# Optimization experiments

Hardware: AMD Instinct MI355X
Metric: run time of the kernel (lower is better)

The kernel has to match this reference:

```python
import jax, jax.numpy as jnp
import numpy as np

B, L, E, H = 2, 2048, 512, 8
D = E // H  # head_dim = 64


def setup_inputs() -> dict:
    key = jax.random.key(0)
    ks = jax.random.split(key, 12)
    s = 0.02
    return {
        "values": jax.random.normal(ks[0], (B, L, E), jnp.float32),
        "keys": jax.random.normal(ks[1], (B, L, E), jnp.float32),
        "query": jax.random.normal(ks[2], (B, L, E), jnp.float32),
        "mask": jax.random.randint(ks[3], (B, 1, L, L), 0, 2, jnp.int32),
        "Wv": jax.random.normal(ks[4], (E, E), jnp.float32) * s,
        "bv": jax.random.normal(ks[5], (E,), jnp.float32) * s,
        "Wk": jax.random.normal(ks[6], (E, E), jnp.float32) * s,
        "bk": jax.random.normal(ks[7], (E,), jnp.float32) * s,
        "Wq": jax.random.normal(ks[8], (E, E), jnp.float32) * s,
        "bq": jax.random.normal(ks[9], (E,), jnp.float32) * s,
        "Wo": jax.random.normal(ks[10], (E, E), jnp.float32) * s,
        "bo": jax.random.normal(ks[11], (E,), jnp.float32) * s,
    }


def reference(values, keys, query, mask, Wv, bv, Wk, bk, Wq, bq, Wo, bo):
    b, lq = query.shape[0], query.shape[1]
    # torch Linear: y = x @ W.T + b
    v = (values @ Wv.T + bv).reshape(b, -1, H, D)
    k = (keys @ Wk.T + bk).reshape(b, -1, H, D)
    q = (query @ Wq.T + bq).reshape(b, lq, H, D)
    energy = jnp.einsum("bqhd,bkhd->bhqk", q, k)  # [B,H,Lq,Lk]
    # mask applied BEFORE the scale, as in the original
    energy = jnp.where(mask == 0, jnp.float32(-1e20), energy)
    # NOTE: scales by sqrt(embed_size), not sqrt(head_dim) (faithful)
    attn = jax.nn.softmax(energy / jnp.sqrt(jnp.float32(E)), axis=3)
    out = jnp.einsum("bhql,blhd->bqhd", attn, v).reshape(b, lq, E)
    return out @ Wo.T + bo
```

## Files before the change

kernel.cpp:

```cpp
#include <hip/hip_runtime.h>
#include <hip/hip_bf16.h>
#include <math.h>

#define BB 2
#define LL 2048
#define EE 512
#define HH 8
#define DD 64
#define MM (BB * LL)
#define LW (LL / 64)

typedef short bf16x8 __attribute__((ext_vector_type(8)));
typedef float f32x4 __attribute__((ext_vector_type(4)));

#define MFMA16(a, b, c) __builtin_amdgcn_mfma_f32_16x16x32_bf16((a), (b), (c), 0, 0, 0)

__device__ __forceinline__ void gl2lds16(const __hip_bfloat16* g, __hip_bfloat16* l) {
    __builtin_amdgcn_global_load_lds(
        (const __attribute__((address_space(1))) unsigned int*)(g),
        (__attribute__((address_space(3))) unsigned int*)(l),
        16, 0, 0);
}

__device__ __forceinline__ uint4 cvt8_bf16(const float4 a, const float4 b) {
    union { __hip_bfloat16 h[8]; uint4 u; } t;
    t.h[0] = __float2bfloat16(a.x); t.h[1] = __float2bfloat16(a.y);
    t.h[2] = __float2bfloat16(a.z); t.h[3] = __float2bfloat16(a.w);
    t.h[4] = __float2bfloat16(b.x); t.h[5] = __float2bfloat16(b.y);
    t.h[6] = __float2bfloat16(b.z); t.h[7] = __float2bfloat16(b.w);
    return t.u;
}

struct PrepArgs {
    const float* xsrc[3];
    __hip_bfloat16* xdst[3];
    const float* wsrc[4];
    __hip_bfloat16* wdst[4];
    const int* mask;
    unsigned long long* mbits;
};

__global__ __launch_bounds__(256) void prep(PrepArgs a) {
    const int blk = blockIdx.x;
    if (blk < 3072) {
        const int t = blk >> 10;
        const int i = ((blk & 1023) * 256 + threadIdx.x) * 8;
        const float* s = a.xsrc[t] + i;
        float4 f0 = *(const float4*)(s);
        float4 f1 = *(const float4*)(s + 4);
        *(uint4*)(a.xdst[t] + i) = cvt8_bf16(f0, f1);
    } else if (blk < 3584) {
        const int r = blk - 3072;
        const int t = r >> 7;
        const int i = ((r & 127) * 256 + threadIdx.x) * 8;
        const float* s = a.wsrc[t] + i;
        float4 f0 = *(const float4*)(s);
        float4 f1 = *(const float4*)(s + 4);
        *(uint4*)(a.wdst[t] + i) = cvt8_bf16(f0, f1);
    } else {
        const size_t idx = (size_t)(blk - 3584) * 256 + threadIdx.x;
        const int m = a.mask[idx];
        const unsigned long long w = __ballot(m != 0);
        if ((threadIdx.x & 63) == 0) a.mbits[idx >> 6] = w;
    }
}

__global__ __launch_bounds__(256) void transpose_v(
    const __hip_bfloat16* __restrict__ vb, __hip_bfloat16* __restrict__ vt) {
    __shared__ __hip_bfloat16 T[64][72];
    const int tid = threadIdx.x;
    const int l0 = blockIdx.x * 64;
    const int h = blockIdx.y;
    const int b = blockIdx.z;
    const int row = tid >> 2;
    const int cg = (tid & 3) * 16;

    const __hip_bfloat16* src = vb + ((size_t)b * LL + l0 + row) * EE + h * DD + cg;
    *(uint4*)&T[row][cg] = *(const uint4*)src;
    *(uint4*)&T[row][cg + 8] = *(const uint4*)(src + 8);
    __syncthreads();

    __hip_bfloat16 t[16];
    #pragma unroll
    for (int e = 0; e < 16; ++e) t[e] = T[cg + e][row];
    __hip_bfloat16* dst = vt + (((size_t)b * HH + h) * DD + row) * LL + l0 + cg;
    *(uint4*)&dst[0] = *(uint4*)&t[0];
    *(uint4*)&dst[8] = *(uint4*)&t[8];
}

struct QKVArgs {
    const __hip_bfloat16* X[3];
    const __hip_bfloat16* W[3];
    const float* bias[3];
    __hip_bfloat16* O[3];
};

__global__ __launch_bounds__(256) void gemm_qkv128(QKVArgs p) {
    __shared__ __hip_bfloat16 As[128 * 32];
    __shared__ __hip_bfloat16 Bs[128 * 32];

    const int z = blockIdx.z;
    const __hip_bfloat16* __restrict__ X = p.X[z];
    const __hip_bfloat16* __restrict__ W = p.W[z];
    const float* __restrict__ bias = p.bias[z];
    __hip_bfloat16* __restrict__ O = p.O[z];
    const float oscale = (z == 0) ? 0.04419417382415922f : 1.0f;

    const int tid = threadIdx.x;
    const int wave = tid >> 6, lane = tid & 63;
    const int l15 = lane & 15, quad = lane >> 4;
    const int wm = (wave >> 1) * 64, wn = (wave & 1) * 64;
    const int m0 = blockIdx.y * 128, n0 = blockIdx.x * 128;

    const int srow = wave * 32 + (lane >> 2);
    const int scol = (lane & 3) * 8;
    const __hip_bfloat16* Ag = X + (size_t)(m0 + srow) * EE + scol;
    const __hip_bfloat16* Bg = W + (size_t)(n0 + srow) * EE + scol;
    __hip_bfloat16* Al = As + wave * 32 * 32;
    __hip_bfloat16* Bl = Bs + wave * 32 * 32;

    f32x4 acc[4][4] = {};

    for (int k0 = 0; k0 < EE; k0 += 32) {
        gl2lds16(Ag + k0, Al);
        gl2lds16(Ag + k0 + (size_t)16 * EE, Al + 16 * 32);
        gl2lds16(Bg + k0, Bl);
        gl2lds16(Bg + k0 + (size_t)16 * EE, Bl + 16 * 32);
        __syncthreads();

        bf16x8 af[4], bfr[4];
        #pragma unroll
        for (int i = 0; i < 4; ++i)
            af[i] = *(const bf16x8*)&As[(wm + i * 16 + l15) * 32 + quad * 8];
        #pragma unroll
        for (int j = 0; j < 4; ++j)
            bfr[j] = *(const bf16x8*)&Bs[(wn + j * 16 + l15) * 32 + quad * 8];
        #pragma unroll
        for (int i = 0; i < 4; ++i)
            #pragma unroll
            for (int j = 0; j < 4; ++j)
                acc[i][j] = MFMA16(af[i], bfr[j], acc[i][j]);
        __syncthreads();
    }

    #pragma unroll
    for (int i = 0; i < 4; ++i)
        #pragma unroll
        for (int j = 0; j < 4; ++j) {
            const int n = n0 + wn + j * 16 + l15;
            const float bv = bias[n];
            #pragma unroll
            for (int reg = 0; reg < 4; ++reg) {
                const int m = m0 + wm + i * 16 + quad * 4 + reg;
                O[(size_t)m * EE + n] = __float2bfloat16((acc[i][j][reg] + bv) * oscale);
            }
        }
}

__global__ __launch_bounds__(256) void gemm_out128(
    const __hip_bfloat16* __restrict__ X, const __hip_bfloat16* __restrict__ W,
    const float* __restrict__ bias, float* __restrict__ C) {
    __shared__ __hip_bfloat16 As[128 * 32];
    __shared__ __hip_bfloat16 Bs[128 * 32];

    const int tid = threadIdx.x;
    const int wave = tid >> 6, lane = tid & 63;
    const int l15 = lane & 15, quad = lane >> 4;
    const int wm = (wave >> 1) * 64, wn = (wave & 1) * 64;
    const int m0 = blockIdx.y * 128, n0 = blockIdx.x * 128;

    const int srow = wave * 32 + (lane >> 2);
    const int scol = (lane & 3) * 8;
    const __hip_bfloat16* Ag = X + (size_t)(m0 + srow) * EE + scol;
    const __hip_bfloat16* Bg = W + (size_t)(n0 + srow) * EE + scol;
    __hip_bfloat16* Al = As + wave * 32 * 32;
    __hip_bfloat16* Bl = Bs + wave * 32 * 32;

    f32x4 acc[4][4] = {};

    for (int k0 = 0; k0 < EE; k0 += 32) {
        gl2lds16(Ag + k0, Al);
        gl2lds16(Ag + k0 + (size_t)16 * EE, Al + 16 * 32);
        gl2lds16(Bg + k0, Bl);
        gl2lds16(Bg + k0 + (size_t)16 * EE, Bl + 16 * 32);
        __syncthreads();

        bf16x8 af[4], bfr[4];
        #pragma unroll
        for (int i = 0; i < 4; ++i)
            af[i] = *(const bf16x8*)&As[(wm + i * 16 + l15) * 32 + quad * 8];
        #pragma unroll
        for (int j = 0; j < 4; ++j)
            bfr[j] = *(const bf16x8*)&Bs[(wn + j * 16 + l15) * 32 + quad * 8];
        #pragma unroll
        for (int i = 0; i < 4; ++i)
            #pragma unroll
            for (int j = 0; j < 4; ++j)
                acc[i][j] = MFMA16(af[i], bfr[j], acc[i][j]);
        __syncthreads();
    }

    #pragma unroll
    for (int i = 0; i < 4; ++i)
        #pragma unroll
        for (int j = 0; j < 4; ++j) {
            const int n = n0 + wn + j * 16 + l15;
            const float bv = bias[n];
            #pragma unroll
            for (int reg = 0; reg < 4; ++reg) {
                const int m = m0 + wm + i * 16 + quad * 4 + reg;
                C[(size_t)m * EE + n] = acc[i][j][reg] + bv;
            }
        }
}

__global__ __launch_bounds__(256) void attn_mfma(
    const __hip_bfloat16* __restrict__ Qb, const __hip_bfloat16* __restrict__ Kb,
    const __hip_bfloat16* __restrict__ vtg, const unsigned long long* __restrict__ mbits,
    __hip_bfloat16* __restrict__ Op) {
    __shared__ __hip_bfloat16 Ks[2][64][72];
    __shared__ __hip_bfloat16 Vs[2][64][72];
    __shared__ __hip_bfloat16 Ps[4][16][72];

    const int tid = threadIdx.x;
    const int wave = tid >> 6;
    const int lane = tid & 63;
    const int l15 = lane & 15;
    const int quad = lane >> 4;
    const int b = blockIdx.z;
    const int h = blockIdx.y;
    const int q0 = blockIdx.x * 64;

    const int srow = tid >> 2;
    const int scg = (tid & 3) * 16;
    const int myq = q0 + wave * 16 + l15;

    bf16x8 qf[2];
    {
        const __hip_bfloat16* qrow = Qb + ((size_t)b * LL + myq) * EE + h * DD;
        qf[0] = *(const bf16x8*)(qrow + quad * 8);
        qf[1] = *(const bf16x8*)(qrow + 32 + quad * 8);
    }

    const __hip_bfloat16* kbase = Kb + ((size_t)b * LL + srow) * EE + h * DD + scg;
    const __hip_bfloat16* vbase = vtg + (((size_t)b * HH + h) * DD + srow) * LL + scg;
    const unsigned long long* mrow = mbits + ((size_t)b * LL + myq) * LW;

    f32x4 o[4] = {};
    float lr0 = 0.f, lr1 = 0.f;

    {
        uint4 k0a = *(const uint4*)(kbase);
        uint4 k0b = *(const uint4*)(kbase + 8);
        uint4 v0a = *(const uint4*)(vbase);
        uint4 v0b = *(const uint4*)(vbase + 8);
        *(uint4*)&Ks[0][srow][scg] = k0a;
        *(uint4*)&Ks[0][srow][scg + 8] = k0b;
        *(uint4*)&Vs[0][srow][scg] = v0a;
        *(uint4*)&Vs[0][srow][scg + 8] = v0b;
    }
    unsigned long long mw_cur = mrow[0];
    __syncthreads();

    for (int t = 0; t < LW; ++t) {
        const int cur = t & 1;
        const int nxt = cur ^ 1;
        const bool more = (t + 1) < LW;

        uint4 ka0, ka1, va0, va1;
        unsigned long long mw_n;
        if (more) {
            const __hip_bfloat16* kn = kbase + (size_t)(t + 1) * 64 * EE;
            const __hip_bfloat16* vn = vbase + (t + 1) * 64;
            ka0 = *(const uint4*)(kn);
            ka1 = *(const uint4*)(kn + 8);
            va0 = *(const uint4*)(vn);
            va1 = *(const uint4*)(vn + 8);
            mw_n = mrow[t + 1];
        }

        f32x4 st[4] = {};
        #pragma unroll
        for (int mt = 0; mt < 4; ++mt) {
            bf16x8 a0 = *(const bf16x8*)&Ks[cur][mt * 16 + l15][quad * 8];
            bf16x8 a1 = *(const bf16x8*)&Ks[cur][mt * 16 + l15][32 + quad * 8];
            st[mt] = MFMA16(a0, qf[0], st[mt]);
            st[mt] = MFMA16(a1, qf[1], st[mt]);
        }

        #pragma unroll
        for (int mt = 0; mt < 4; ++mt) {
            float p[4];
            #pragma unroll
            for (int reg = 0; reg < 4; ++reg) {
                const bool live = (mw_cur >> (mt * 16 + quad * 4 + reg)) & 1ull;
                const float e = __expf(st[mt][reg]);
                p[reg] = live ? e : 0.f;
            }
            lr0 += p[0] + p[1];
            lr1 += p[2] + p[3];
            union { __hip_bfloat16 h[4]; ushort4 v; } pk;
            pk.h[0] = __float2bfloat16(p[0]);
            pk.h[1] = __float2bfloat16(p[1]);
            pk.h[2] = __float2bfloat16(p[2]);
            pk.h[3] = __float2bfloat16(p[3]);
            *(ushort4*)&Ps[wave][l15][mt * 16 + quad * 4] = pk.v;
        }

        bf16x8 pa0 = *(const bf16x8*)&Ps[wave][l15][quad * 8];
        bf16x8 pa1 = *(const bf16x8*)&Ps[wave][l15][32 + quad * 8];
        #pragma unroll
        for (int nt = 0; nt < 4; ++nt) {
            bf16x8 vb0 = *(const bf16x8*)&Vs[cur][nt * 16 + l15][quad * 8];
            bf16x8 vb1 = *(const bf16x8*)&Vs[cur][nt * 16 + l15][32 + quad * 8];
            o[nt] = MFMA16(pa0, vb0, o[nt]);
            o[nt] = MFMA16(pa1, vb1, o[nt]);
        }

        if (more) {
            *(uint4*)&Ks[nxt][srow][scg] = ka0;
            *(uint4*)&Ks[nxt][srow][scg + 8] = ka1;
            *(uint4*)&Vs[nxt][srow][scg] = va0;
            *(uint4*)&Vs[nxt][srow][scg + 8] = va1;
            mw_cur = mw_n;
        }
        __syncthreads();
    }

    float lrun = lr0 + lr1;
    lrun += __shfl_xor(lrun, 16);
    lrun += __shfl_xor(lrun, 32);
    const float linv = 1.f / lrun;
    float linvR[4];
    #pragma unroll
    for (int reg = 0; reg < 4; ++reg)
        linvR[reg] = __shfl(linv, quad * 4 + reg);

    __hip_bfloat16* Ob = Op + ((size_t)b * LL + q0 + wave * 16) * EE + h * DD;
    #pragma unroll
    for (int nt = 0; nt < 4; ++nt)
        #pragma unroll
        for (int reg = 0; reg < 4; ++reg) {
            const int qrow = quad * 4 + reg;
            Ob[(size_t)qrow * EE + nt * 16 + l15] =
                __float2bfloat16(o[nt][reg] * linvR[reg]);
        }
}

extern "C" void kernel_launch(void* const* d_in, const int* in_sizes, int n_in,
                              void* d_out, int out_size, void* d_ws, size_t ws_size,
                              hipStream_t stream) {
    const float* values = (const float*)d_in[0];
    const float* keys   = (const float*)d_in[1];
    const float* query  = (const float*)d_in[2];
    const int*   mask   = (const int*)d_in[3];
    const float* Wv = (const float*)d_in[4];
    const float* bv = (const float*)d_in[5];
    const float* Wk = (const float*)d_in[6];
    const float* bk = (const float*)d_in[7];
    const float* Wq = (const float*)d_in[8];
    const float* bq = (const float*)d_in[9];
    const float* Wo = (const float*)d_in[10];
    const float* bo = (const float*)d_in[11];
    float* out = (float*)d_out;

    const size_t XS = (size_t)MM * EE * 2;
    const size_t WS = (size_t)EE * EE * 2;
    char* w = (char*)d_ws;
    __hip_bfloat16* xq  = (__hip_bfloat16*)(w);
    __hip_bfloat16* xk  = (__hip_bfloat16*)(w + XS);
    __hip_bfloat16* xv  = (__hip_bfloat16*)(w + 2 * XS);
    __hip_bfloat16* qb  = (__hip_bfloat16*)(w + 3 * XS);
    __hip_bfloat16* kb  = (__hip_bfloat16*)(w + 4 * XS);
    __hip_bfloat16* vb  = (__hip_bfloat16*)(w + 5 * XS);
    __hip_bfloat16* vtg = (__hip_bfloat16*)(w + 6 * XS);
    __hip_bfloat16* aob = (__hip_bfloat16*)(w + 7 * XS);
    __hip_bfloat16* wqb = (__hip_bfloat16*)(w + 8 * XS);
    __hip_bfloat16* wkb = (__hip_bfloat16*)(w + 8 * XS + WS);
    __hip_bfloat16* wvb = (__hip_bfloat16*)(w + 8 * XS + 2 * WS);
    __hip_bfloat16* wob = (__hip_bfloat16*)(w + 8 * XS + 3 * WS);
    unsigned long long* mbits = (unsigned long long*)(w + 8 * XS + 4 * WS);

    PrepArgs pa;
    pa.xsrc[0] = query; pa.xsrc[1] = keys; pa.xsrc[2] = values;
    pa.xdst[0] = xq;    pa.xdst[1] = xk;   pa.xdst[2] = xv;
    pa.wsrc[0] = Wq; pa.wsrc[1] = Wk; pa.wsrc[2] = Wv; pa.wsrc[3] = Wo;
    pa.wdst[0] = wqb; pa.wdst[1] = wkb; pa.wdst[2] = wvb; pa.wdst[3] = wob;
    pa.mask = mask; pa.mbits = mbits;

    QKVArgs qa;
    qa.X[0] = xq;  qa.X[1] = xk;  qa.X[2] = xv;
    qa.W[0] = wqb; qa.W[1] = wkb; qa.W[2] = wvb;
    qa.bias[0] = bq; qa.bias[1] = bk; qa.bias[2] = bv;
    qa.O[0] = qb;  qa.O[1] = kb;  qa.O[2] = vb;

    prep<<<36352, 256, 0, stream>>>(pa);
    gemm_qkv128<<<dim3(EE / 128, MM / 128, 3), 256, 0, stream>>>(qa);
    transpose_v<<<dim3(LL / 64, HH, BB), 256, 0, stream>>>(vb, vtg);
    attn_mfma<<<dim3(LL / 64, HH, BB), 256, 0, stream>>>(qb, kb, vtg, mbits, aob);
    gemm_out128<<<dim3(EE / 128, MM / 128), 256, 0, stream>>>(aob, wob, bo, out);
}
```

Before: 189.8 us.

## Double-buffer GEMMs and attention K/V via direct LDS loads, use exp2

Rewrites both projection GEMMs with 64x128 tiles, BK=64, and double-buffered global-to-LDS async loads, so loads of the next tile overlap MFMA work and more blocks are launched. The attention kernel switches K/V staging from register round-trips to direct global_load_lds into a split-half LDS layout. The Q scale now folds in log2(e), so the softmax can use a native exp2 instead of expf. The mask-packing blocks each handle 16 rows to cut the prep grid size. This trades more LDS per block and a different bank-access pattern for fewer register copies and better latency hiding.

```diff
diff --git a/kernel.cpp b/kernel.cpp
--- a/kernel.cpp
+++ b/kernel.cpp
@@ -14,6 +14,14 @@
 typedef float f32x4 __attribute__((ext_vector_type(4)));
 
 #define MFMA16(a, b, c) __builtin_amdgcn_mfma_f32_16x16x32_bf16((a), (b), (c), 0, 0, 0)
+
+#if __has_builtin(__builtin_amdgcn_exp2f)
+#define EXP2(x) __builtin_amdgcn_exp2f(x)
+#else
+#define EXP2(x) exp2f(x)
+#endif
+
+#define QSCALE 0.0637587146f
 
 __device__ __forceinline__ void gl2lds16(const __hip_bfloat16* g, __hip_bfloat16* l) {
     __builtin_amdgcn_global_load_lds(
@@ -58,10 +66,14 @@
         float4 f1 = *(const float4*)(s + 4);
         *(uint4*)(a.wdst[t] + i) = cvt8_bf16(f0, f1);
     } else {
-        const size_t idx = (size_t)(blk - 3584) * 256 + threadIdx.x;
-        const int m = a.mask[idx];
-        const unsigned long long w = __ballot(m != 0);
-        if ((threadIdx.x & 63) == 0) a.mbits[idx >> 6] = w;
+        const int mb = blk - 3584;
+        #pragma unroll
+        for (int r = 0; r < 16; ++r) {
+            const size_t idx = ((size_t)mb * 16 + r) * 256 + threadIdx.x;
+            const int m = a.mask[idx];
+            const unsigned long long w = __ballot(m != 0);
+            if ((threadIdx.x & 63) == 0) a.mbits[idx >> 6] = w;
+        }
     }
 }
 
@@ -95,120 +107,130 @@
     __hip_bfloat16* O[3];
 };
 
-__global__ __launch_bounds__(256) void gemm_qkv128(QKVArgs p) {
-    __shared__ __hip_bfloat16 As[128 * 32];
-    __shared__ __hip_bfloat16 Bs[128 * 32];
+__global__ __launch_bounds__(256) void gemm_qkv(QKVArgs p) {
+    __shared__ __hip_bfloat16 As[2][2][64][32];
+    __shared__ __hip_bfloat16 Bs[2][2][128][32];
 
     const int z = blockIdx.z;
     const __hip_bfloat16* __restrict__ X = p.X[z];
     const __hip_bfloat16* __restrict__ W = p.W[z];
     const float* __restrict__ bias = p.bias[z];
     __hip_bfloat16* __restrict__ O = p.O[z];
-    const float oscale = (z == 0) ? 0.04419417382415922f : 1.0f;
+    const float oscale = (z == 0) ? QSCALE : 1.0f;
 
     const int tid = threadIdx.x;
     const int wave = tid >> 6, lane = tid & 63;
     const int l15 = lane & 15, quad = lane >> 4;
-    const int wm = (wave >> 1) * 64, wn = (wave & 1) * 64;
-    const int m0 = blockIdx.y * 128, n0 = blockIdx.x * 128;
-
-    const int srow = wave * 32 + (lane >> 2);
-    const int scol = (lane & 3) * 8;
-    const __hip_bfloat16* Ag = X + (size_t)(m0 + srow) * EE + scol;
-    const __hip_bfloat16* Bg = W + (size_t)(n0 + srow) * EE + scol;
-    __hip_bfloat16* Al = As + wave * 32 * 32;
-    __hip_bfloat16* Bl = Bs + wave * 32 * 32;
-
-    f32x4 acc[4][4] = {};
-
-    for (int k0 = 0; k0 < EE; k0 += 32) {
-        gl2lds16(Ag + k0, Al);
-        gl2lds16(Ag + k0 + (size_t)16 * EE, Al + 16 * 32);
-        gl2lds16(Bg + k0, Bl);
-        gl2lds16(Bg + k0 + (size_t)16 * EE, Bl + 16 * 32);
-        __syncthreads();
-
-        bf16x8 af[4], bfr[4];
-        #pragma unroll
-        for (int i = 0; i < 4; ++i)
-            af[i] = *(const bf16x8*)&As[(wm + i * 16 + l15) * 32 + quad * 8];
-        #pragma unroll
-        for (int j = 0; j < 4; ++j)
-            bfr[j] = *(const bf16x8*)&Bs[(wn + j * 16 + l15) * 32 + quad * 8];
-        #pragma unroll
-        for (int i = 0; i < 4; ++i)
-            #pragma unroll
-            for (int j = 0; j < 4; ++j)
-                acc[i][j] = MFMA16(af[i], bfr[j], acc[i][j]);
+    const int wn = wave * 32;
+    const int m0 = blockIdx.y * 64, n0 = blockIdx.x * 128;
+
+    const int lr = lane >> 2;
+    const int lc = (lane & 3) * 8;
+    const __hip_bfloat16* Ax = X + (size_t)(m0 + wave * 16 + lr) * EE + lc;
+    const __hip_bfloat16* Bx = W + (size_t)(n0 + wave * 32 + lr) * EE + lc;
+
+    f32x4 acc[4][2] = {};
+
+    #define STAGE_G(buf, k0)                                                   \
+        gl2lds16(Ax + (k0),           &As[buf][0][wave * 16][0]);              \
+        gl2lds16(Ax + (k0) + 32,      &As[buf][1][wave * 16][0]);              \
+        gl2lds16(Bx + (k0),           &Bs[buf][0][wave * 32][0]);              \
+        gl2lds16(Bx + (k0) + 32,      &Bs[buf][1][wave * 32][0]);              \
+        gl2lds16(Bx + (k0) + 16 * EE,      &Bs[buf][0][wave * 32 + 16][0]);    \
+        gl2lds16(Bx + (k0) + 16 * EE + 32, &Bs[buf][1][wave * 32 + 16][0]);
+
+    STAGE_G(0, 0);
+    __syncthreads();
+
+    for (int kt = 0; kt < 8; ++kt) {
+        const int cur = kt & 1;
+        if (kt < 7) { STAGE_G(cur ^ 1, (kt + 1) * 64); }
+
+        #pragma unroll
+        for (int c = 0; c < 2; ++c) {
+            bf16x8 af[4], bf2[2];
+            #pragma unroll
+            for (int i = 0; i < 4; ++i)
+                af[i] = *(const bf16x8*)&As[cur][c][i * 16 + l15][quad * 8];
+            #pragma unroll
+            for (int j = 0; j < 2; ++j)
+                bf2[j] = *(const bf16x8*)&Bs[cur][c][wn + j * 16 + l15][quad * 8];
+            #pragma unroll
+            for (int i = 0; i < 4; ++i)
+                #pragma unroll
+                for (int j = 0; j < 2; ++j)
+                    acc[i][j] = MFMA16(af[i], bf2[j], acc[i][j]);
+        }
         __syncthreads();
     }
 
     #pragma unroll
     for (int i = 0; i < 4; ++i)
         #pragma unroll
-        for (int j = 0; j < 4; ++j) {
+        for (int j = 0; j < 2; ++j) {
             const int n = n0 + wn + j * 16 + l15;
             const float bv = bias[n];
             #pragma unroll
             for (int reg = 0; reg < 4; ++reg) {
-                const int m = m0 + wm + i * 16 + quad * 4 + reg;
+                const int m = m0 + i * 16 + quad * 4 + reg;
                 O[(size_t)m * EE + n] = __float2bfloat16((acc[i][j][reg] + bv) * oscale);
             }
         }
 }
 
-__global__ __launch_bounds__(256) void gemm_out128(
+__global__ __launch_bounds__(256) void gemm_out(
     const __hip_bfloat16* __restrict__ X, const __hip_bfloat16* __restrict__ W,
     const float* __restrict__ bias, float* __restrict__ C) {
-    __shared__ __hip_bfloat16 As[128 * 32];
-    __shared__ __hip_bfloat16 Bs[128 * 32];
+    __shared__ __hip_bfloat16 As[2][2][64][32];
+    __shared__ __hip_bfloat16 Bs[2][2][128][32];
 
     const int tid = threadIdx.x;
     const int wave = tid >> 6, lane = tid & 63;
     const int l15 = lane & 15, quad = lane >> 4;
-    const int wm = (wave >> 1) * 64, wn = (wave & 1) * 64;
-    const int m0 = blockIdx.y * 128, n0 = blockIdx.x * 128;
-
-    const int srow = wave * 32 + (lane >> 2);
-    const int scol = (lane & 3) * 8;
-    const __hip_bfloat16* Ag = X + (size_t)(m0 + srow) * EE + scol;
-    const __hip_bfloat16* Bg = W + (size_t)(n0 + srow) * EE + scol;
-    __hip_bfloat16* Al = As + wave * 32 * 32;
-    __hip_bfloat16* Bl = Bs + wave * 32 * 32;
-
-    f32x4 acc[4][4] = {};
-
-    for (int k0 = 0; k0 < EE; k0 += 32) {
-        gl2lds16(Ag + k0, Al);
-        gl2lds16(Ag + k0 + (size_t)16 * EE, Al + 16 * 32);
-        gl2lds16(Bg + k0, Bl);
-        gl2lds16(Bg + k0 + (size_t)16 * EE, Bl + 16 * 32);
-        __syncthreads();
-
-        bf16x8 af[4], bfr[4];
-        #pragma unroll
-        for (int i = 0; i < 4; ++i)
-            af[i] = *(const bf16x8*)&As[(wm + i * 16 + l15) * 32 + quad * 8];
-        #pragma unroll
-        for (int j = 0; j < 4; ++j)
-            bfr[j] = *(const bf16x8*)&Bs[(wn + j * 16 + l15) * 32 + quad * 8];
-        #pragma unroll
-        for (int i = 0; i < 4; ++i)
-            #pragma unroll
-            for (int j = 0; j < 4; ++j)
-                acc[i][j] = MFMA16(af[i], bfr[j], acc[i][j]);
+    const int wn = wave * 32;
+    const int m0 = blockIdx.y * 64, n0 = blockIdx.x * 128;
+
+    const int lr = lane >> 2;
+    const int lc = (lane & 3) * 8;
+    const __hip_bfloat16* Ax = X + (size_t)(m0 + wave * 16 + lr) * EE + lc;
+    const __hip_bfloat16* Bx = W + (size_t)(n0 + wave * 32 + lr) * EE + lc;
+
+    f32x4 acc[4][2] = {};
+
+    STAGE_G(0, 0);
+    __syncthreads();
+
+    for (int kt = 0; kt < 8; ++kt) {
+        const int cur = kt & 1;
+        if (kt < 7) { STAGE_G(cur ^ 1, (kt + 1) * 64); }
+
+        #pragma unroll
+        for (int c = 0; c < 2; ++c) {
+            bf16x8 af[4], bf2[2];
+            #pragma unroll
+            for (int i = 0; i < 4; ++i)
+                af[i] = *(const bf16x8*)&As[cur][c][i * 16 + l15][quad * 8];
+            #pragma unroll
+            for (int j = 0; j < 2; ++j)
+                bf2[j] = *(const bf16x8*)&Bs[cur][c][wn + j * 16 + l15][quad * 8];
+            #pragma unroll
+            for (int i = 0; i < 4; ++i)
+                #pragma unroll
+                for (int j = 0; j < 2; ++j)
+                    acc[i][j] = MFMA16(af[i], bf2[j], acc[i][j]);
+        }
         __syncthreads();
     }
 
     #pragma unroll
     for (int i = 0; i < 4; ++i)
         #pragma unroll
-        for (int j = 0; j < 4; ++j) {
+        for (int j = 0; j < 2; ++j) {
             const int n = n0 + wn + j * 16 + l15;
             const float bv = bias[n];
             #pragma unroll
             for (int reg = 0; reg < 4; ++reg) {
-                const int m = m0 + wm + i * 16 + quad * 4 + reg;
+                const int m = m0 + i * 16 + quad * 4 + reg;
                 C[(size_t)m * EE + n] = acc[i][j][reg] + bv;
             }
         }
@@ -218,8 +240,8 @@
     const __hip_bfloat16* __restrict__ Qb, const __hip_bfloat16* __restrict__ Kb,
     const __hip_bfloat16* __restrict__ vtg, const unsigned long long* __restrict__ mbits,
     __hip_bfloat16* __restrict__ Op) {
-    __shared__ __hip_bfloat16 Ks[2][64][72];
-    __shared__ __hip_bfloat16 Vs[2][64][72];
+    __shared__ __hip_bfloat16 Ks[2][2][64][32];
+    __shared__ __hip_bfloat16 Vs[2][2][64][32];
     __shared__ __hip_bfloat16 Ps[4][16][72];
 
     const int tid = threadIdx.x;
@@ -230,9 +252,6 @@
     const int b = blockIdx.z;
     const int h = blockIdx.y;
     const int q0 = blockIdx.x * 64;
-
-    const int srow = tid >> 2;
-    const int scg = (tid & 3) * 16;
     const int myq = q0 + wave * 16 + l15;
 
     bf16x8 qf[2];
@@ -242,48 +261,38 @@
         qf[1] = *(const bf16x8*)(qrow + 32 + quad * 8);
     }
 
-    const __hip_bfloat16* kbase = Kb + ((size_t)b * LL + srow) * EE + h * DD + scg;
-    const __hip_bfloat16* vbase = vtg + (((size_t)b * HH + h) * DD + srow) * LL + scg;
+    const int lr = lane >> 2;
+    const int lc = (lane & 3) * 8;
+    const __hip_bfloat16* Kx = Kb + ((size_t)b * LL + wave * 16 + lr) * EE + h * DD + lc;
+    const __hip_bfloat16* Vx = vtg + (((size_t)b * HH + h) * DD + wave * 16 + lr) * LL + lc;
     const unsigned long long* mrow = mbits + ((size_t)b * LL + myq) * LW;
 
     f32x4 o[4] = {};
     float lr0 = 0.f, lr1 = 0.f;
 
-    {
-        uint4 k0a = *(const uint4*)(kbase);
-        uint4 k0b = *(const uint4*)(kbase + 8);
-        uint4 v0a = *(const uint4*)(vbase);
-        uint4 v0b = *(const uint4*)(vbase + 8);
-        *(uint4*)&Ks[0][srow][scg] = k0a;
-        *(uint4*)&Ks[0][srow][scg + 8] = k0b;
-        *(uint4*)&Vs[0][srow][scg] = v0a;
-        *(uint4*)&Vs[0][srow][scg + 8] = v0b;
-    }
+    #define STAGE_KV(buf, k0)                                                  \
+        gl2lds16(Kx + (size_t)(k0) * EE,      &Ks[buf][0][wave * 16][0]);      \
+        gl2lds16(Kx + (size_t)(k0) * EE + 32, &Ks[buf][1][wave * 16][0]);      \
+        gl2lds16(Vx + (k0),                   &Vs[buf][0][wave * 16][0]);      \
+        gl2lds16(Vx + (k0) + 32,              &Vs[buf][1][wave * 16][0]);
+
+    STAGE_KV(0, 0);
     unsigned long long mw_cur = mrow[0];
     __syncthreads();
 
     for (int t = 0; t < LW; ++t) {
         const int cur = t & 1;
-        const int nxt = cur ^ 1;
-        const bool more = (t + 1) < LW;
-
-        uint4 ka0, ka1, va0, va1;
         unsigned long long mw_n;
-        if (more) {
-            const __hip_bfloat16* kn = kbase + (size_t)(t + 1) * 64 * EE;
-            const __hip_bfloat16* vn = vbase + (t + 1) * 64;
-            ka0 = *(const uint4*)(kn);
-            ka1 = *(const uint4*)(kn + 8);
-            va0 = *(const uint4*)(vn);
-            va1 = *(const uint4*)(vn + 8);
+        if (t + 1 < LW) {
+            STAGE_KV(cur ^ 1, (t + 1) * 64);
             mw_n = mrow[t + 1];
         }
 
         f32x4 st[4] = {};
         #pragma unroll
         for (int mt = 0; mt < 4; ++mt) {
-            bf16x8 a0 = *(const bf16x8*)&Ks[cur][mt * 16 + l15][quad * 8];
-            bf16x8 a1 = *(const bf16x8*)&Ks[cur][mt * 16 + l15][32 + quad * 8];
+            bf16x8 a0 = *(const bf16x8*)&Ks[cur][0][mt * 16 + l15][quad * 8];
+            bf16x8 a1 = *(const bf16x8*)&Ks[cur][1][mt * 16 + l15][quad * 8];
             st[mt] = MFMA16(a0, qf[0], st[mt]);
             st[mt] = MFMA16(a1, qf[1], st[mt]);
         }
@@ -294,16 +303,16 @@
             #pragma unroll
             for (int reg = 0; reg < 4; ++reg) {
                 const bool live = (mw_cur >> (mt * 16 + quad * 4 + reg)) & 1ull;
-                const float e = __expf(st[mt][reg]);
+                const float e = EXP2(st[mt][reg]);
                 p[reg] = live ? e : 0.f;
             }
             lr0 += p[0] + p[1];
             lr1 += p[2] + p[3];
-            union { __hip_bfloat16 h[4]; ushort4 v; } pk;
-            pk.h[0] = __float2bfloat16(p[0]);
-            pk.h[1] = __float2bfloat16(p[1]);
-            pk.h[2] = __float2bfloat16(p[2]);
-            pk.h[3] = __float2bfloat16(p[3]);
+            union { __hip_bfloat16 hh[4]; ushort4 v; } pk;
+            pk.hh[0] = __float2bfloat16(p[0]);
+            pk.hh[1] = __float2bfloat16(p[1]);
+            pk.hh[2] = __float2bfloat16(p[2]);
+            pk.hh[3] = __float2bfloat16(p[3]);
             *(ushort4*)&Ps[wave][l15][mt * 16 + quad * 4] = pk.v;
         }
 
@@ -311,19 +320,13 @@
         bf16x8 pa1 = *(const bf16x8*)&Ps[wave][l15][32 + quad * 8];
         #pragma unroll
         for (int nt = 0; nt < 4; ++nt) {
-            bf16x8 vb0 = *(const bf16x8*)&Vs[cur][nt * 16 + l15][quad * 8];
-            bf16x8 vb1 = *(const bf16x8*)&Vs[cur][nt * 16 + l15][32 + quad * 8];
+            bf16x8 vb0 = *(const bf16x8*)&Vs[cur][0][nt * 16 + l15][quad * 8];
+            bf16x8 vb1 = *(const bf16x8*)&Vs[cur][1][nt * 16 + l15][quad * 8];
             o[nt] = MFMA16(pa0, vb0, o[nt]);
             o[nt] = MFMA16(pa1, vb1, o[nt]);
         }
 
-        if (more) {
-            *(uint4*)&Ks[nxt][srow][scg] = ka0;
-            *(uint4*)&Ks[nxt][srow][scg + 8] = ka1;
-            *(uint4*)&Vs[nxt][srow][scg] = va0;
-            *(uint4*)&Vs[nxt][srow][scg + 8] = va1;
-            mw_cur = mw_n;
-        }
+        if (t + 1 < LW) mw_cur = mw_n;
         __syncthreads();
     }
 
@@ -394,9 +397,9 @@
     qa.bias[0] = bq; qa.bias[1] = bk; qa.bias[2] = bv;
     qa.O[0] = qb;  qa.O[1] = kb;  qa.O[2] = vb;
 
-    prep<<<36352, 256, 0, stream>>>(pa);
-    gemm_qkv128<<<dim3(EE / 128, MM / 128, 3), 256, 0, stream>>>(qa);
+    prep<<<5632, 256, 0, stream>>>(pa);
+    gemm_qkv<<<dim3(EE / 128, MM / 64, 3), 256, 0, stream>>>(qa);
     transpose_v<<<dim3(LL / 64, HH, BB), 256, 0, stream>>>(vb, vtg);
     attn_mfma<<<dim3(LL / 64, HH, BB), 256, 0, stream>>>(qb, kb, vtg, mbits, aob);
-    gemm_out128<<<dim3(EE / 128, MM / 128), 256, 0, stream>>>(aob, wob, bo, out);
-}
+    gemm_out<<<dim3(EE / 128, MM / 64), 256, 0, stream>>>(aob, wob, bo, out);
+}
```

New measurement: 190.4 us. No clear change (+0.3%).

## Drop LDS staging in projection GEMMs, use exp2 softmax, batch mask packing

Applied to the files above, without the earlier changes.

The QKV and output GEMMs no longer stage through LDS with global_load_lds and barriers. Each wave now loads its bf16 fragments straight from global memory into registers, using 128x64 block tiles that give more blocks. The attention kernel folds log2(e) into the Q scale so it can use the hardware exp2 instead of __expf. It also shrinks the LDS row padding from 72 to 68 and keeps a single running sum. The prep kernel packs 16 mask rows per block, which cuts the launch from 36352 blocks to 5632. Reading directly from global gives up LDS reuse and leans on the L2 cache, and the 68-element padding may change LDS bank conflicts.

```diff
diff --git a/kernel.cpp b/kernel.cpp
--- a/kernel.cpp
+++ b/kernel.cpp
@@ -15,12 +15,13 @@
 
 #define MFMA16(a, b, c) __builtin_amdgcn_mfma_f32_16x16x32_bf16((a), (b), (c), 0, 0, 0)
 
-__device__ __forceinline__ void gl2lds16(const __hip_bfloat16* g, __hip_bfloat16* l) {
-    __builtin_amdgcn_global_load_lds(
-        (const __attribute__((address_space(1))) unsigned int*)(g),
-        (__attribute__((address_space(3))) unsigned int*)(l),
-        16, 0, 0);
-}
+#if __has_builtin(__builtin_amdgcn_exp2f)
+#define EXP2(x) __builtin_amdgcn_exp2f(x)
+#else
+#define EXP2(x) exp2f(x)
+#endif
+
+#define QSCALE 0.0637587146f
 
 __device__ __forceinline__ uint4 cvt8_bf16(const float4 a, const float4 b) {
     union { __hip_bfloat16 h[8]; uint4 u; } t;
@@ -58,10 +59,14 @@
         float4 f1 = *(const float4*)(s + 4);
         *(uint4*)(a.wdst[t] + i) = cvt8_bf16(f0, f1);
     } else {
-        const size_t idx = (size_t)(blk - 3584) * 256 + threadIdx.x;
-        const int m = a.mask[idx];
-        const unsigned long long w = __ballot(m != 0);
-        if ((threadIdx.x & 63) == 0) a.mbits[idx >> 6] = w;
+        const int mb = blk - 3584;
+        #pragma unroll
+        for (int r = 0; r < 16; ++r) {
+            const size_t idx = ((size_t)mb * 16 + r) * 256 + threadIdx.x;
+            const int m = a.mask[idx];
+            const unsigned long long w = __ballot(m != 0);
+            if ((threadIdx.x & 63) == 0) a.mbits[idx >> 6] = w;
+        }
     }
 }
 
@@ -95,120 +100,98 @@
     __hip_bfloat16* O[3];
 };
 
-__global__ __launch_bounds__(256) void gemm_qkv128(QKVArgs p) {
-    __shared__ __hip_bfloat16 As[128 * 32];
-    __shared__ __hip_bfloat16 Bs[128 * 32];
-
+__global__ __launch_bounds__(256) void gemm_qkv(QKVArgs p) {
     const int z = blockIdx.z;
     const __hip_bfloat16* __restrict__ X = p.X[z];
     const __hip_bfloat16* __restrict__ W = p.W[z];
     const float* __restrict__ bias = p.bias[z];
     __hip_bfloat16* __restrict__ O = p.O[z];
-    const float oscale = (z == 0) ? 0.04419417382415922f : 1.0f;
+    const float oscale = (z == 0) ? QSCALE : 1.0f;
 
     const int tid = threadIdx.x;
     const int wave = tid >> 6, lane = tid & 63;
     const int l15 = lane & 15, quad = lane >> 4;
-    const int wm = (wave >> 1) * 64, wn = (wave & 1) * 64;
-    const int m0 = blockIdx.y * 128, n0 = blockIdx.x * 128;
-
-    const int srow = wave * 32 + (lane >> 2);
-    const int scol = (lane & 3) * 8;
-    const __hip_bfloat16* Ag = X + (size_t)(m0 + srow) * EE + scol;
-    const __hip_bfloat16* Bg = W + (size_t)(n0 + srow) * EE + scol;
-    __hip_bfloat16* Al = As + wave * 32 * 32;
-    __hip_bfloat16* Bl = Bs + wave * 32 * 32;
-
-    f32x4 acc[4][4] = {};
-
+    const int mw = blockIdx.y * 128 + wave * 32;
+    const int n0 = blockIdx.x * 64;
+
+    const __hip_bfloat16* Arow = X + (size_t)(mw + l15) * EE + quad * 8;
+    const __hip_bfloat16* Brow = W + (size_t)(n0 + l15) * EE + quad * 8;
+
+    f32x4 acc[2][4] = {};
+
+    #pragma unroll 4
     for (int k0 = 0; k0 < EE; k0 += 32) {
-        gl2lds16(Ag + k0, Al);
-        gl2lds16(Ag + k0 + (size_t)16 * EE, Al + 16 * 32);
-        gl2lds16(Bg + k0, Bl);
-        gl2lds16(Bg + k0 + (size_t)16 * EE, Bl + 16 * 32);
-        __syncthreads();
-
-        bf16x8 af[4], bfr[4];
-        #pragma unroll
-        for (int i = 0; i < 4; ++i)
-            af[i] = *(const bf16x8*)&As[(wm + i * 16 + l15) * 32 + quad * 8];
-        #pragma unroll
-        for (int j = 0; j < 4; ++j)
-            bfr[j] = *(const bf16x8*)&Bs[(wn + j * 16 + l15) * 32 + quad * 8];
-        #pragma unroll
-        for (int i = 0; i < 4; ++i)
-            #pragma unroll
-            for (int j = 0; j < 4; ++j)
-                acc[i][j] = MFMA16(af[i], bfr[j], acc[i][j]);
-        __syncthreads();
-    }
-
-    #pragma unroll
-    for (int i = 0; i < 4; ++i)
+        bf16x8 a0 = *(const bf16x8*)(Arow + k0);
+        bf16x8 a1 = *(const bf16x8*)(Arow + (size_t)16 * EE + k0);
+        bf16x8 b0 = *(const bf16x8*)(Brow + k0);
+        bf16x8 b1 = *(const bf16x8*)(Brow + (size_t)16 * EE + k0);
+        bf16x8 b2 = *(const bf16x8*)(Brow + (size_t)32 * EE + k0);
+        bf16x8 b3 = *(const bf16x8*)(Brow + (size_t)48 * EE + k0);
+        acc[0][0] = MFMA16(a0, b0, acc[0][0]);
+        acc[0][1] = MFMA16(a0, b1, acc[0][1]);
+        acc[0][2] = MFMA16(a0, b2, acc[0][2]);
+        acc[0][3] = MFMA16(a0, b3, acc[0][3]);
+        acc[1][0] = MFMA16(a1, b0, acc[1][0]);
+        acc[1][1] = MFMA16(a1, b1, acc[1][1]);
+        acc[1][2] = MFMA16(a1, b2, acc[1][2]);
+        acc[1][3] = MFMA16(a1, b3, acc[1][3]);
+    }
+
+    #pragma unroll
+    for (int i = 0; i < 2; ++i)
         #pragma unroll
         for (int j = 0; j < 4; ++j) {
-            const int n = n0 + wn + j * 16 + l15;
+            const int n = n0 + j * 16 + l15;
             const float bv = bias[n];
             #pragma unroll
             for (int reg = 0; reg < 4; ++reg) {
-                const int m = m0 + wm + i * 16 + quad * 4 + reg;
+                const int m = mw + i * 16 + quad * 4 + reg;
                 O[(size_t)m * EE + n] = __float2bfloat16((acc[i][j][reg] + bv) * oscale);
             }
         }
 }
 
-__global__ __launch_bounds__(256) void gemm_out128(
+__global__ __launch_bounds__(256) void gemm_out(
     const __hip_bfloat16* __restrict__ X, const __hip_bfloat16* __restrict__ W,
     const float* __restrict__ bias, float* __restrict__ C) {
-    __shared__ __hip_bfloat16 As[128 * 32];
-    __shared__ __hip_bfloat16 Bs[128 * 32];
-
     const int tid = threadIdx.x;
     const int wave = tid >> 6, lane = tid & 63;
     const int l15 = lane & 15, quad = lane >> 4;
-    const int wm = (wave >> 1) * 64, wn = (wave & 1) * 64;
-    const int m0 = blockIdx.y * 128, n0 = blockIdx.x * 128;
-
-    const int srow = wave * 32 + (lane >> 2);
-    const int scol = (lane & 3) * 8;
-    const __hip_bfloat16* Ag = X + (size_t)(m0 + srow) * EE + scol;
-    const __hip_bfloat16* Bg = W + (size_t)(n0 + srow) * EE + scol;
-    __hip_bfloat16* Al = As + wave * 32 * 32;
-    __hip_bfloat16* Bl = Bs + wave * 32 * 32;
-
-    f32x4 acc[4][4] = {};
-
+    const int mw = blockIdx.y * 128 + wave * 32;
+    const int n0 = blockIdx.x * 64;
+
+    const __hip_bfloat16* Arow = X + (size_t)(mw + l15) * EE + quad * 8;
+    const __hip_bfloat16* Brow = W + (size_t)(n0 + l15) * EE + quad * 8;
+
+    f32x4 acc[2][4] = {};
+
+    #pragma unroll 4
     for (int k0 = 0; k0 < EE; k0 += 32) {
-        gl2lds16(Ag + k0, Al);
-        gl2lds16(Ag + k0 + (size_t)16 * EE, Al + 16 * 32);
-        gl2lds16(Bg + k0, Bl);
-        gl2lds16(Bg + k0 + (size_t)16 * EE, Bl + 16 * 32);
-        __syncthreads();
-
-        bf16x8 af[4], bfr[4];
-        #pragma unroll
-        for (int i = 0; i < 4; ++i)
-            af[i] = *(const bf16x8*)&As[(wm + i * 16 + l15) * 32 + quad * 8];
-        #pragma unroll
-        for (int j = 0; j < 4; ++j)
-            bfr[j] = *(const bf16x8*)&Bs[(wn + j * 16 + l15) * 32 + quad * 8];
-        #pragma unroll
-        for (int i = 0; i < 4; ++i)
-            #pragma unroll
-            for (int j = 0; j < 4; ++j)
-                acc[i][j] = MFMA16(af[i], bfr[j], acc[i][j]);
-        __syncthreads();
-    }
-
-    #pragma unroll
-    for (int i = 0; i < 4; ++i)
+        bf16x8 a0 = *(const bf16x8*)(Arow + k0);
+        bf16x8 a1 = *(const bf16x8*)(Arow + (size_t)16 * EE + k0);
+        bf16x8 b0 = *(const bf16x8*)(Brow + k0);
+        bf16x8 b1 = *(const bf16x8*)(Brow + (size_t)16 * EE + k0);
+        bf16x8 b2 = *(const bf16x8*)(Brow + (size_t)32 * EE + k0);
+        bf16x8 b3 = *(const bf16x8*)(Brow + (size_t)48 * EE + k0);
+        acc[0][0] = MFMA16(a0, b0, acc[0][0]);
+        acc[0][1] = MFMA16(a0, b1, acc[0][1]);
+        acc[0][2] = MFMA16(a0, b2, acc[0][2]);
+        acc[0][3] = MFMA16(a0, b3, acc[0][3]);
+        acc[1][0] = MFMA16(a1, b0, acc[1][0]);
+        acc[1][1] = MFMA16(a1, b1, acc[1][1]);
+        acc[1][2] = MFMA16(a1, b2, acc[1][2]);
+        acc[1][3] = MFMA16(a1, b3, acc[1][3]);
+    }
+
+    #pragma unroll
+    for (int i = 0; i < 2; ++i)
         #pragma unroll
         for (int j = 0; j < 4; ++j) {
-            const int n = n0 + wn + j * 16 + l15;
+            const int n = n0 + j * 16 + l15;
             const float bv = bias[n];
             #pragma unroll
             for (int reg = 0; reg < 4; ++reg) {
-                const int m = m0 + wm + i * 16 + quad * 4 + reg;
+                const int m = mw + i * 16 + quad * 4 + reg;
                 C[(size_t)m * EE + n] = acc[i][j][reg] + bv;
             }
         }
@@ -218,9 +201,9 @@
     const __hip_bfloat16* __restrict__ Qb, const __hip_bfloat16* __restrict__ Kb,
     const __hip_bfloat16* __restrict__ vtg, const unsigned long long* __restrict__ mbits,
     __hip_bfloat16* __restrict__ Op) {
-    __shared__ __hip_bfloat16 Ks[2][64][72];
-    __shared__ __hip_bfloat16 Vs[2][64][72];
-    __shared__ __hip_bfloat16 Ps[4][16][72];
+    __shared__ __hip_bfloat16 Ks[2][64][68];
+    __shared__ __hip_bfloat16 Vs[2][64][68];
+    __shared__ __hip_bfloat16 Ps[4][16][68];
 
     const int tid = threadIdx.x;
     const int wave = tid >> 6;
@@ -230,10 +213,10 @@
     const int b = blockIdx.z;
     const int h = blockIdx.y;
     const int q0 = blockIdx.x * 64;
+    const int myq = q0 + wave * 16 + l15;
 
     const int srow = tid >> 2;
     const int scg = (tid & 3) * 16;
-    const int myq = q0 + wave * 16 + l15;
 
     bf16x8 qf[2];
     {
@@ -247,7 +230,7 @@
     const unsigned long long* mrow = mbits + ((size_t)b * LL + myq) * LW;
 
     f32x4 o[4] = {};
-    float lr0 = 0.f, lr1 = 0.f;
+    float lrun = 0.f;
 
     {
         uint4 k0a = *(const uint4*)(kbase);
@@ -294,16 +277,15 @@
             #pragma unroll
             for (int reg = 0; reg < 4; ++reg) {
                 const bool live = (mw_cur >> (mt * 16 + quad * 4 + reg)) & 1ull;
-                const float e = __expf(st[mt][reg]);
+                const float e = EXP2(st[mt][reg]);
                 p[reg] = live ? e : 0.f;
+                lrun += p[reg];
             }
-            lr0 += p[0] + p[1];
-            lr1 += p[2] + p[3];
-            union { __hip_bfloat16 h[4]; ushort4 v; } pk;
-            pk.h[0] = __float2bfloat16(p[0]);
-            pk.h[1] = __float2bfloat16(p[1]);
-            pk.h[2] = __float2bfloat16(p[2]);
-            pk.h[3] = __float2bfloat16(p[3]);
+            union { __hip_bfloat16 hh[4]; ushort4 v; } pk;
+            pk.hh[0] = __float2bfloat16(p[0]);
+            pk.hh[1] = __float2bfloat16(p[1]);
+            pk.hh[2] = __float2bfloat16(p[2]);
+            pk.hh[3] = __float2bfloat16(p[3]);
             *(ushort4*)&Ps[wave][l15][mt * 16 + quad * 4] = pk.v;
         }
 
@@ -327,7 +309,6 @@
         __syncthreads();
     }
 
-    float lrun = lr0 + lr1;
     lrun += __shfl_xor(lrun, 16);
     lrun += __shfl_xor(lrun, 32);
     const float linv = 1.f / lrun;
@@ -394,9 +375,9 @@
     qa.bias[0] = bq; qa.bias[1] = bk; qa.bias[2] = bv;
     qa.O[0] = qb;  qa.O[1] = kb;  qa.O[2] = vb;
 
-    prep<<<36352, 256, 0, stream>>>(pa);
-    gemm_qkv128<<<dim3(EE / 128, MM / 128, 3), 256, 0, stream>>>(qa);
+    prep<<<5632, 256, 0, stream>>>(pa);
+    gemm_qkv<<<dim3(EE / 64, MM / 128, 3), 256, 0, stream>>>(qa);
     transpose_v<<<dim3(LL / 64, HH, BB), 256, 0, stream>>>(vb, vtg);
     attn_mfma<<<dim3(LL / 64, HH, BB), 256, 0, stream>>>(qb, kb, vtg, mbits, aob);
-    gemm_out128<<<dim3(EE / 128, MM / 128), 256, 0, stream>>>(aob, wob, bo, out);
-}
+    gemm_out<<<dim3(EE / 64, MM / 128), 256, 0, stream>>>(aob, wob, bo, out);
+}
```

Result: slower. 207.8 us (+9.5%).
